# Kernel optimization log

Hardware: AMD Instinct MI355X
Metric: run time of the kernel (lower is better)

## Reference

```python
import jax, jax.numpy as jnp
import numpy as np

VOCAB = 50000
EMBED = 256
BATCH = 16384
NUM_SAMPLED = 4096


def _log_uniform_prob(ids):
    # P(c) = (log(c+2) - log(c+1)) / log(V+1), the log-uniform sampler distribution
    ids = ids.astype(jnp.float32)
    return (jnp.log(ids + 2.0) - jnp.log(ids + 1.0)) / jnp.log(VOCAB + 1.0)


def _expected_count(ids, num_sampled):
    # unique log-uniform sampler expected count: 1 - (1 - p)^num_tries, num_tries ~= num_sampled
    p = _log_uniform_prob(ids)
    return -jnp.expm1(num_sampled * jnp.log1p(-p))


def _sigmoid_xent(logits, labels):
    # stable sigmoid cross-entropy: max(x,0) - x*z + log(1 + exp(-|x|))
    return jnp.maximum(logits, 0.0) - logits * labels + jnp.log1p(jnp.exp(-jnp.abs(logits)))


def setup_inputs() -> dict:
    key = jax.random.key(0)
    k1, k2, k3, k4 = jax.random.split(key, 4)
    embedding = jax.random.normal(k1, (BATCH, EMBED), dtype=jnp.float32)
    target_words = jax.random.randint(k2, (BATCH, 1), 0, VOCAB, dtype=jnp.int64 if jax.config.jax_enable_x64 else jnp.int32)
    sampled_ids = jax.random.randint(k3, (NUM_SAMPLED,), 0, VOCAB, dtype=jnp.int64 if jax.config.jax_enable_x64 else jnp.int32)
    # truncated-normal init with stddev 1/sqrt(embed_size), matching TruncatedNormal
    nce_weight = (jax.random.truncated_normal(k4, -2.0, 2.0, (VOCAB, EMBED), dtype=jnp.float32)
                  * (1.0 / EMBED ** 0.5))
    nce_bias = jnp.zeros((VOCAB,), dtype=jnp.float32)
    return {"embedding": embedding, "target_words": target_words,
            "sampled_ids": sampled_ids, "nce_weight": nce_weight, "nce_bias": nce_bias}


def reference(embedding, target_words, sampled_ids, nce_weight, nce_bias):
    num_sampled = sampled_ids.shape[0]
    labels = target_words[:, 0]                       # [B]

    # gather true-class rows and compute true logits (subtract_log_q=True in tf.nn.nce_loss)
    w_true = nce_weight[labels]                       # [B, D]
    true_logits = (jnp.sum(embedding * w_true, axis=-1) + nce_bias[labels]
                   - jnp.log(_expected_count(labels, num_sampled)))          # [B]

    # gather sampled rows and compute sampled logits
    w_samp = nce_weight[sampled_ids]                  # [S, D]
    sampled_logits = (jnp.einsum('bd,sd->bs', embedding, w_samp) + nce_bias[sampled_ids]
                      - jnp.log(_expected_count(sampled_ids, num_sampled)))  # [B, S]

    # sigmoid cross-entropy: true label 1, sampled labels 0; sum per example, mean over batch
    per_example = _sigmoid_xent(true_logits, 1.0) + jnp.sum(_sigmoid_xent(sampled_logits, 0.0), axis=-1)
    return jnp.mean(per_example)
```

## Files before the change

kernel.cpp:

```cpp
#include <hip/hip_runtime.h>
#include <cstdint>
#include <cstddef>

#define VOCAB 50000
#define EMBED 256
#define BATCH 16384
#define NSAMP 4096

typedef float f32x4 __attribute__((ext_vector_type(4)));
typedef int   i32x8 __attribute__((ext_vector_type(8)));


__device__ __forceinline__ float log_expected_count(int id) {
    float idf = (float)id;
    float p = log1pf(1.0f / (idf + 1.0f)) / logf((float)(VOCAB + 1));
    return __logf(-expm1f((float)NSAMP * log1pf(-p)));
}

__device__ __forceinline__ float softplus_f(float x) {
    float v = __expf(-fabsf(x));
    float p = fmaf(v, 0.03215845f, -0.13606275f);
    p = fmaf(v, p, 0.28947478f);
    p = fmaf(v, p, -0.49190896f);
    p = fmaf(v, p, 0.99949556f);
    return fmaxf(x, 0.0f) + v * p;
}

__device__ __forceinline__ int pk4_fp8(float a, float b, float c, float d) {
    int v = __builtin_amdgcn_cvt_pk_fp8_f32(a, b, 0, false);
    v = __builtin_amdgcn_cvt_pk_fp8_f32(c, d, v, true);
    return v;
}



__global__ __launch_bounds__(256) void k_prep(
        const float* __restrict__ E, const int* __restrict__ tgt,
        const int* __restrict__ sids, const float* __restrict__ W,
        const float* __restrict__ bias,
        unsigned char* __restrict__ EF, unsigned char* __restrict__ BF,
        float* __restrict__ badj, double* __restrict__ pTrue)
{
    const int blk = blockIdx.x, tid = threadIdx.x;
    const int wave = tid >> 6, lane = tid & 63;

    if (blk < 1024) {
        float tsum = 0.0f;
        #pragma unroll
        for (int i = 0; i < 4; ++i) {
            int b = (blk * 4 + wave) + 4096 * i;
            int label = tgt[b];
            float4 e  = ((const float4*)(E + (size_t)b * EMBED))[lane];
            float4 wv = ((const float4*)(W + (size_t)label * EMBED))[lane];
            int pk = pk4_fp8(e.x, e.y, e.z, e.w);
            *(int*)(EF + ((b >> 4) * 4096 + (lane >> 3) * 512
                          + (b & 15) * 32 + (lane & 7) * 4)) = pk;
            float d = e.x * wv.x + e.y * wv.y + e.z * wv.z + e.w * wv.w;
            #pragma unroll
            for (int off = 32; off > 0; off >>= 1) d += __shfl_down(d, off, 64);
            if (lane == 0) {
                float tl = d + bias[label] - log_expected_count(label);
                tsum += softplus_f(-tl);
            }
        }
        __shared__ float ts[4];
        if (lane == 0) ts[wave] = tsum;
        __syncthreads();
        if (tid == 0) pTrue[blk] = (double)((ts[0] + ts[1]) + (ts[2] + ts[3]));
    } else {
        #pragma unroll
        for (int i = 0; i < 4; ++i) {
            int task = (blk - 1024) * 256 + tid + 16384 * i;
            int s = task >> 4, p = task & 15;
            int sid = sids[s];
            const float4* wr = (const float4*)(W + (size_t)sid * EMBED + p * 16);
            float4 w0 = wr[0], w1 = wr[1], w2 = wr[2], w3 = wr[3];
            int4 o;
            o.x = pk4_fp8(w0.x * 16.0f, w0.y * 16.0f, w0.z * 16.0f, w0.w * 16.0f);
            o.y = pk4_fp8(w1.x * 16.0f, w1.y * 16.0f, w1.z * 16.0f, w1.w * 16.0f);
            o.z = pk4_fp8(w2.x * 16.0f, w2.y * 16.0f, w2.z * 16.0f, w2.w * 16.0f);
            o.w = pk4_fp8(w3.x * 16.0f, w3.y * 16.0f, w3.z * 16.0f, w3.w * 16.0f);
            *(int4*)(BF + ((s >> 4) * 4096 + (p >> 1) * 512
                           + (s & 15) * 32 + (p & 1) * 16)) = o;
            if (p == 0) badj[s] = bias[sid] - log_expected_count(sid);
        }
    }
}

__global__ __launch_bounds__(256, 2) void k_gemm(
        const unsigned char* __restrict__ EF,
        const unsigned char* __restrict__ BF,
        const float* __restrict__ badj,
        double* __restrict__ pGemm)
{
    const int tid  = threadIdx.x;
    const int wave = tid >> 6;
    const int lane = tid & 63;
    const int rg   = blockIdx.x >> 3;
    const int cg   = blockIdx.x & 7;
    const int ag0  = rg * 16 + wave * 4;
    const int r16  = lane & 15;

    i32x8 af[2][4];
    #pragma unroll
    for (int s = 0; s < 2; ++s)
        #pragma unroll
        for (int mi = 0; mi < 4; ++mi)
            af[s][mi] = *(const i32x8*)(EF + (size_t)(ag0 + mi) * 4096
                                        + s * 2048 + lane * 32);

    float lsum = 0.0f;
    #pragma unroll 1
    for (int j = 0; j < 8; ++j) {
        const int bg0 = cg * 32 + j * 4;
        i32x8 bf[2][4];
        #pragma unroll
        for (int s = 0; s < 2; ++s)
            #pragma unroll
            for (int ni = 0; ni < 4; ++ni)
                bf[s][ni] = *(const i32x8*)(BF + (size_t)(bg0 + ni) * 4096
                                            + s * 2048 + lane * 32);

        f32x4 acc[4][4] = {};
        #pragma unroll
        for (int s = 0; s < 2; ++s)
            #pragma unroll
            for (int mi = 0; mi < 4; ++mi)
                #pragma unroll
                for (int ni = 0; ni < 4; ++ni)
                    acc[mi][ni] = __builtin_amdgcn_mfma_scale_f32_16x16x128_f8f6f4(
                        af[s][mi], bf[s][ni], acc[mi][ni],
                        0, 0,
                        0, 0x7F7F7F7F,
                        0, 0x7B7B7B7B);

        const int cbase = cg * 512 + j * 64 + r16;
        #pragma unroll
        for (int ni = 0; ni < 4; ++ni) {
            float ba = badj[cbase + ni * 16];
            #pragma unroll
            for (int mi = 0; mi < 4; ++mi)
                #pragma unroll
                for (int r = 0; r < 4; ++r)
                    lsum += softplus_f(acc[mi][ni][r] + ba);
        }
    }

    #pragma unroll
    for (int off = 32; off > 0; off >>= 1) lsum += __shfl_down(lsum, off, 64);
    __shared__ float wsum[4];
    if (lane == 0) wsum[wave] = lsum;
    __syncthreads();
    if (tid == 0)
        pGemm[blockIdx.x] = (double)((wsum[0] + wsum[1]) + (wsum[2] + wsum[3]));
}

__global__ __launch_bounds__(256) void k_final(
        const double* __restrict__ pTrue, const double* __restrict__ pGemm,
        float* __restrict__ out)
{
    const int tid = threadIdx.x, wave = tid >> 6, lane = tid & 63;
    double s = 0.0;
    for (int i = tid; i < 1024; i += 256) s += pTrue[i];
    for (int i = tid; i < 512; i += 256) s += pGemm[i];
    #pragma unroll
    for (int off = 32; off > 0; off >>= 1) s += __shfl_down(s, off, 64);
    __shared__ double wsum[4];
    if (lane == 0) wsum[wave] = s;
    __syncthreads();
    if (tid == 0)
        out[0] = (float)(((wsum[0] + wsum[1]) + (wsum[2] + wsum[3]))
                         * (1.0 / (double)BATCH));
}


extern "C" void kernel_launch(void* const* d_in, const int* in_sizes, int n_in,
                              void* d_out, int out_size, void* d_ws, size_t ws_size,
                              hipStream_t stream) {
    const float* emb  = (const float*)d_in[0];
    const int*   tgt  = (const int*)d_in[1];
    const int*   sids = (const int*)d_in[2];
    const float* W    = (const float*)d_in[3];
    const float* bias = (const float*)d_in[4];
    float* out = (float*)d_out;

    char* ws = (char*)d_ws;
    double*        pTrue = (double*)ws;
    double*        pGemm = (double*)(ws + 8192);
    float*         badj  = (float*)(ws + 40960);
    unsigned char* BF    = (unsigned char*)(ws + 57344);
    unsigned char* EF    = (unsigned char*)(ws + 57344 + 1048576);

    hipLaunchKernelGGL(k_prep, dim3(1088), dim3(256), 0, stream,
                       emb, tgt, sids, W, bias, EF, BF, badj, pTrue);
    hipLaunchKernelGGL(k_gemm, dim3(512), dim3(256), 0, stream,
                       EF, BF, badj, pGemm);
    hipLaunchKernelGGL(k_final, dim3(1), dim3(256), 0, stream,
                       pTrue, pGemm, out);
}
```

Baseline: 142.2 us.

## Double-buffer B fragment loads and split MFMA tile into halves in GEMM

The GEMM loop now prefetches the next B fragments into a second register buffer while computing the current one, hiding global load latency behind the MFMAs. Each iteration's MFMA work is split into two halves of the M tiles, so the accumulators shrink and softplus on one half can interleave with MFMAs on the other. log_expected_count swaps library log1p/expm1 for fast intrinsics plus a truncated series. That last part trades some accuracy for cheaper math in the prep kernel. The extra buffer raises register pressure under the 2-blocks-per-SIMD launch bound.

```diff
diff --git a/kernel.cpp b/kernel.cpp
--- a/kernel.cpp
+++ b/kernel.cpp
@@ -12,9 +12,12 @@
 
 
 __device__ __forceinline__ float log_expected_count(int id) {
-    float idf = (float)id;
-    float p = log1pf(1.0f / (idf + 1.0f)) / logf((float)(VOCAB + 1));
-    return __logf(-expm1f((float)NSAMP * log1pf(-p)));
+    float u = 1.0f / ((float)id + 1.0f);
+    float a = __logf(1.0f + u);
+    float p = a * 0.09242324f;
+    float ser = p * (1.0f + p * (0.5f + p * (0.33333333f + p * (0.25f + p * 0.2f))));
+    float q = -(float)NSAMP * ser;
+    return __logf(1.0f - __expf(q));
 }
 
 __device__ __forceinline__ float softplus_f(float x) {
@@ -110,40 +113,54 @@
                                         + s * 2048 + lane * 32);
 
     float lsum = 0.0f;
-    #pragma unroll 1
-    for (int j = 0; j < 8; ++j) {
+
+    auto load_b = [&](i32x8 (&bf)[2][4], int j) {
         const int bg0 = cg * 32 + j * 4;
-        i32x8 bf[2][4];
         #pragma unroll
         for (int s = 0; s < 2; ++s)
             #pragma unroll
             for (int ni = 0; ni < 4; ++ni)
                 bf[s][ni] = *(const i32x8*)(BF + (size_t)(bg0 + ni) * 4096
                                             + s * 2048 + lane * 32);
-
-        f32x4 acc[4][4] = {};
-        #pragma unroll
-        for (int s = 0; s < 2; ++s)
-            #pragma unroll
-            for (int mi = 0; mi < 4; ++mi)
+    };
+
+    auto compute_j = [&](const i32x8 (&bf)[2][4], int j) {
+        float ba[4];
+        #pragma unroll
+        for (int ni = 0; ni < 4; ++ni)
+            ba[ni] = badj[cg * 512 + j * 64 + ni * 16 + r16];
+        #pragma unroll
+        for (int half = 0; half < 2; ++half) {
+            f32x4 acc[2][4] = {};
+            #pragma unroll
+            for (int s = 0; s < 2; ++s)
                 #pragma unroll
-                for (int ni = 0; ni < 4; ++ni)
-                    acc[mi][ni] = __builtin_amdgcn_mfma_scale_f32_16x16x128_f8f6f4(
-                        af[s][mi], bf[s][ni], acc[mi][ni],
-                        0, 0,
-                        0, 0x7F7F7F7F,
-                        0, 0x7B7B7B7B);
-
-        const int cbase = cg * 512 + j * 64 + r16;
-        #pragma unroll
-        for (int ni = 0; ni < 4; ++ni) {
-            float ba = badj[cbase + ni * 16];
-            #pragma unroll
-            for (int mi = 0; mi < 4; ++mi)
+                for (int mi = 0; mi < 2; ++mi)
+                    #pragma unroll
+                    for (int ni = 0; ni < 4; ++ni)
+                        acc[mi][ni] = __builtin_amdgcn_mfma_scale_f32_16x16x128_f8f6f4(
+                            af[s][half * 2 + mi], bf[s][ni], acc[mi][ni],
+                            0, 0,
+                            0, 0x7F7F7F7F,
+                            0, 0x7B7B7B7B);
+            #pragma unroll
+            for (int ni = 0; ni < 4; ++ni)
                 #pragma unroll
-                for (int r = 0; r < 4; ++r)
-                    lsum += softplus_f(acc[mi][ni][r] + ba);
+                for (int mi = 0; mi < 2; ++mi)
+                    #pragma unroll
+                    for (int r = 0; r < 4; ++r)
+                        lsum += softplus_f(acc[mi][ni][r] + ba[ni]);
         }
+    };
+
+    i32x8 b0[2][4], b1[2][4];
+    load_b(b0, 0);
+    #pragma unroll 1
+    for (int jj = 0; jj < 4; ++jj) {
+        load_b(b1, jj * 2 + 1);
+        compute_j(b0, jj * 2);
+        if (jj < 3) load_b(b0, jj * 2 + 2);
+        compute_j(b1, jj * 2 + 1);
     }
 
     #pragma unroll
```

After: 155.7 us. 1.09x slower.
